# Optimization experiments

Measured on AMD Instinct MI355X. Metric: run time of the kernel, lower is better.

Reference implementation:

```python
import jax, jax.numpy as jnp
import numpy as np

N, E, H, FE, FV, L, FL, FO = 20000, 320000, 256, 64, 64, 4, 1024, 1


def setup_inputs() -> dict:
    key = jax.random.key(0)
    ks = jax.random.split(key, 28)
    s = 0.05
    rn = lambda k, shp: jax.random.normal(k, shp, jnp.float32) * s
    inp = {
        'x': jax.random.normal(ks[0], (N, FV), jnp.float32),
        'edge_attr': jax.random.normal(ks[1], (E, FE), jnp.float32),
        'edge_index': jax.random.randint(ks[2], (2, E), 0, N, jnp.int64) if False else jax.random.randint(ks[2], (2, E), 0, N),
        'ew': rn(ks[3], (H, FE)), 'eb': rn(ks[4], (H,)),
        'vw': rn(ks[5], (H, FV)), 'vb': rn(ks[6], (H,)),
        'Le_w': rn(ks[7], (L, H, H)), 'Le_b': rn(ks[8], (L, H)),
        'Lv_w': rn(ks[9], (L, H, H)), 'Lv_b': rn(ks[10], (L, H)),
        'bne_g': jnp.ones((L, H), jnp.float32), 'bne_b': jnp.zeros((L, H), jnp.float32),
        'bnv_g': jnp.ones((L, H), jnp.float32), 'bnv_b': jnp.zeros((L, H), jnp.float32),
        'gru_wih': rn(ks[11], (L, 3 * H, H)), 'gru_whh': rn(ks[12], (L, 3 * H, H)),
        'gru_bih': rn(ks[13], (L, 3 * H)), 'gru_bhh': rn(ks[14], (L, 3 * H)),
        'fin_w': rn(ks[15], (FL, H)), 'fin_b': rn(ks[16], (FL,)),
        'out_w': rn(ks[17], (FO, FL)), 'out_b': rn(ks[18], (FO,)),
    }
    return inp


def _bn(x, g, b):
    # BatchNorm1d, training-mode batch statistics (biased variance), eps=1e-5
    m = x.mean(axis=0)
    v = x.var(axis=0)
    return (x - m) * jax.lax.rsqrt(v + 1e-5) * g + b


def _forward(x, edge_attr, edge_index, ew, eb, vw, vb, Le_w, Le_b, Lv_w, Lv_b,
             bne_g, bne_b, bnv_g, bnv_b, gru_wih, gru_whh, gru_bih, gru_bhh,
             fin_w, fin_b, out_w, out_b):
    n_nodes = x.shape[0]
    num_layers = Le_w.shape[0]
    src, dst = edge_index[0], edge_index[1]
    seg = jnp.concatenate([src, dst])  # each edge contributes to both endpoints
    e_in = edge_attr @ ew.T + eb       # [E, H]
    v_in = x @ vw.T + vb               # [N, H]
    for k in range(num_layers):
        e = e_in @ Le_w[k].T + Le_b[k]
        vp = v_in @ Lv_w[k].T + Lv_b[k]
        ep = jax.nn.relu(_bn(e + vp[src] + vp[dst], bne_g[k], bne_b[k]))  # [E, H]
        # scatter-max of incident edge features into each vertex
        vie = jax.ops.segment_max(jnp.concatenate([ep, ep], axis=0), seg,
                                  num_segments=n_nodes)
        vie = jnp.where(jnp.isfinite(vie), vie, 0.0)  # isolated vertices -> 0
        # single-step GRU: input vie, hidden v_in
        gi = vie @ gru_wih[k].T + gru_bih[k]
        gh = v_in @ gru_whh[k].T + gru_bhh[k]
        ir, iz, ig = jnp.split(gi, 3, axis=1)
        hr, hz, hg = jnp.split(gh, 3, axis=1)
        r = jax.nn.sigmoid(ir + hr)
        z = jax.nn.sigmoid(iz + hz)
        n = jnp.tanh(ig + r * hg)
        h = (1.0 - z) * n + z * v_in
        v_c = jax.nn.relu(_bn(h, bnv_g[k], bnv_b[k]))
        v_in = v_c + v_in
        e_in = ep + e_in
    e_fin = e_in @ fin_w.T + fin_b
    return e_fin @ out_w.T + out_b  # [E, 1]


def reference(x, edge_attr, edge_index, ew, eb, vw, vb, Le_w, Le_b, Lv_w, Lv_b,
              bne_g, bne_b, bnv_g, bnv_b, gru_wih, gru_whh, gru_bih, gru_bhh,
              fin_w, fin_b, out_w, out_b):
    return _forward(x, edge_attr, edge_index, ew, eb, vw, vb, Le_w, Le_b, Lv_w,
                    Lv_b, bne_g, bne_b, bnv_g, bnv_b, gru_wih, gru_whh,
                    gru_bih, gru_bhh, fin_w, fin_b, out_w, out_b)
```

## Files before the change

### kernel.cpp

```cpp
#include <hip/hip_runtime.h>
#include <stdint.h>

constexpr int N  = 20000;
constexpr int E  = 320000;
constexpr int H  = 256;
constexpr int FEAT = 64;
constexpr int NL = 4;
constexpr int FL = 1024;
constexpr int NB_E = E / 32;

typedef unsigned short u16;
typedef short bf16x8 __attribute__((ext_vector_type(8)));
typedef float f32x4 __attribute__((ext_vector_type(4)));

__device__ __forceinline__ float bf2f(u16 u) {
    union { uint32_t i; float f; } v; v.i = ((uint32_t)u) << 16; return v.f;
}
__device__ __forceinline__ u16 f2bf(float f) {
    union { uint32_t i; float f; } v; v.f = f;
    uint32_t r = v.i + 0x7FFFu + ((v.i >> 16) & 1u);
    return (u16)(r >> 16);
}
__device__ __forceinline__ float sigmf(float x) { return 1.f / (1.f + __expf(-x)); }
__device__ __forceinline__ float tanhf_(float x) { return 2.f / (1.f + __expf(-2.f * x)) - 1.f; }

__device__ __forceinline__ unsigned int encf(float x) {
    unsigned int u = __float_as_uint(x);
    return (u & 0x80000000u) ? ~u : (u | 0x80000000u);
}
__device__ __forceinline__ float decf(unsigned int k) {
    unsigned int u = (k & 0x80000000u) ? (k ^ 0x80000000u) : ~k;
    return __uint_as_float(u);
}

template <bool W16>
__device__ __forceinline__ bf16x8 ldb(const u16* wb, const float* wf, size_t off) {
    if constexpr (W16) {
        return *(const bf16x8*)(wb + off);
    } else {
        float4 b0 = *(const float4*)(wf + off);
        float4 b1 = *(const float4*)(wf + off + 4);
        bf16x8 r;
        r[0] = (short)f2bf(b0.x); r[1] = (short)f2bf(b0.y);
        r[2] = (short)f2bf(b0.z); r[3] = (short)f2bf(b0.w);
        r[4] = (short)f2bf(b1.x); r[5] = (short)f2bf(b1.y);
        r[6] = (short)f2bf(b1.z); r[7] = (short)f2bf(b1.w);
        return r;
    }
}

__global__ void k_fuse_final(const float* __restrict__ fin_w, const float* __restrict__ fin_b,
                             const float* __restrict__ out_w, const float* __restrict__ out_b,
                             float* __restrict__ w_fo) {
    int h = threadIdx.x;
    float acc = 0.f;
    for (int f = 0; f < FL; ++f) acc = fmaf(out_w[f], fin_w[(size_t)f * H + h], acc);
    w_fo[h] = acc;
    if (h == 0) {
        float b = 0.f;
        for (int f = 0; f < FL; ++f) b = fmaf(out_w[f], fin_b[f], b);
        w_fo[H] = b + out_b[0];
    }
}

__global__ void k_cvt_w(const float* __restrict__ w, u16* __restrict__ o, int n4) {
    int i = blockIdx.x * 256 + threadIdx.x;
    if (i < n4) {
        float4 v = *(const float4*)(w + (size_t)i * 4);
        *(ushort4*)(o + (size_t)i * 4) = make_ushort4(f2bf(v.x), f2bf(v.y), f2bf(v.z), f2bf(v.w));
    }
}

__global__ void k_zero_int(int* __restrict__ p, int n) {
    int i = blockIdx.x * 256 + threadIdx.x;
    if (i < n) p[i] = 0;
}
__global__ void k_zero_f64(double* __restrict__ p, int n) {
    int i = blockIdx.x * 256 + threadIdx.x;
    if (i < n) p[i] = 0.0;
}
__global__ void k_hist2(const int* __restrict__ src, const int* __restrict__ dst,
                        int* __restrict__ curS, int* __restrict__ curD) {
    int e = blockIdx.x * 256 + threadIdx.x;
    if (e < E) { atomicAdd(&curS[src[e]], 1); atomicAdd(&curD[dst[e]], 1); }
}
__global__ void k_scan(int* __restrict__ cur) {
    __shared__ int cs[256];
    int t = threadIdx.x;
    constexpr int CH = (N + 255) / 256;
    int beg = t * CH, end = min(beg + CH, N);
    int s = 0;
    for (int i = beg; i < end; ++i) s += cur[i];
    cs[t] = s;
    __syncthreads();
    for (int off = 1; off < 256; off <<= 1) {
        int v = cs[t];
        int u = (t >= off) ? cs[t - off] : 0;
        __syncthreads();
        cs[t] = v + u;
        __syncthreads();
    }
    int run = (t > 0) ? cs[t - 1] : 0;
    for (int i = beg; i < end; ++i) { int d = cur[i]; cur[i] = run; run += d; }
}
__global__ void k_fill_perm(const int* __restrict__ src, const int* __restrict__ dst,
                            int* __restrict__ curS, int* __restrict__ curD,
                            int4* __restrict__ adjS, int4* __restrict__ sd2, int* __restrict__ pos) {
    int e = blockIdx.x * 256 + threadIdx.x;
    if (e < E) {
        int s = src[e], d = dst[e];
        int q = atomicAdd(&curD[d], 1);
        sd2[q] = make_int4(s, d, e, 0);
        pos[e] = q;
        int p = atomicAdd(&curS[s], 1);
        adjS[p] = make_int4(q, s, d, s);
    }
}
__global__ void k_fill_u32(unsigned int* __restrict__ p, unsigned int val) {
    size_t i = ((size_t)blockIdx.x * 256 + threadIdx.x) * 4;
    uint4 v = make_uint4(val, val, val, val);
    *(uint4*)(p + i) = v;
}

template <bool W16>
__global__ __launch_bounds__(256, 3) void k_proj_mfma(
    const float* __restrict__ A, const u16* __restrict__ wb, const float* __restrict__ wf,
    const float* __restrict__ bias, u16* __restrict__ C, int M, const int* __restrict__ perm)
{
    __shared__ u16 As[64][72];
    int t = threadIdx.x;
    int row0 = blockIdx.x * 64;
    int r = t >> 2, q = t & 3;
    if (row0 + r < M) {
        const float* gp = A + (size_t)(row0 + r) * FEAT + q * 16;
#pragma unroll
        for (int i = 0; i < 4; ++i) {
            float4 v = *(const float4*)(gp + i * 4);
            *(ushort4*)&As[r][q * 16 + i * 4] = make_ushort4(f2bf(v.x), f2bf(v.y), f2bf(v.z), f2bf(v.w));
        }
    } else {
#pragma unroll
        for (int i = 0; i < 4; ++i) *(ushort4*)&As[r][q * 16 + i * 4] = make_ushort4(0, 0, 0, 0);
    }
    __syncthreads();
    int w = t >> 6, l = t & 63, lane16 = l & 15, quad = l >> 4;
    f32x4 acc[4][4];
#pragma unroll
    for (int i = 0; i < 4; ++i)
#pragma unroll
        for (int j = 0; j < 4; ++j) acc[i][j] = (f32x4){0.f, 0.f, 0.f, 0.f};
#pragma unroll
    for (int k0 = 0; k0 < FEAT; k0 += 32) {
        bf16x8 a[4], b[4];
#pragma unroll
        for (int mt = 0; mt < 4; ++mt)
            a[mt] = *(const bf16x8*)&As[mt * 16 + lane16][k0 + quad * 8];
#pragma unroll
        for (int nt = 0; nt < 4; ++nt)
            b[nt] = ldb<W16>(wb, wf, (size_t)(w * 16 + nt * 64 + lane16) * FEAT + k0 + quad * 8);
#pragma unroll
        for (int mt = 0; mt < 4; ++mt)
#pragma unroll
            for (int nt = 0; nt < 4; ++nt)
                acc[mt][nt] = __builtin_amdgcn_mfma_f32_16x16x32_bf16(a[mt], b[nt], acc[mt][nt], 0, 0, 0);
    }
#pragma unroll
    for (int nt = 0; nt < 4; ++nt) {
        int col = w * 16 + nt * 64 + lane16;
        float bv = bias[col];
#pragma unroll
        for (int mt = 0; mt < 4; ++mt)
#pragma unroll
            for (int reg = 0; reg < 4; ++reg) {
                int row = mt * 16 + quad * 4 + reg;
                if (row0 + row < M) {
                    int pr = perm ? perm[row0 + row] : row0 + row;
                    C[(size_t)pr * H + col] = f2bf(acc[mt][nt][reg] + bv);
                }
            }
    }
}

template <bool W16>
__global__ __launch_bounds__(256, 2) void k_node_mfma(
    const u16* __restrict__ A, const u16* __restrict__ wb, const float* __restrict__ wf,
    u16* __restrict__ C)
{
    __shared__ u16 As[64][264];
    int t = threadIdx.x;
    int row0 = blockIdx.x * 64;
    int rows = min(64, N - row0);
    int r = t >> 2, q = t & 3;
    if (r < rows) {
        const u16* gp = A + (size_t)(row0 + r) * H + q * 64;
#pragma unroll
        for (int i = 0; i < 16; ++i)
            *(ushort4*)&As[r][q * 64 + i * 4] = *(const ushort4*)(gp + i * 4);
    } else {
#pragma unroll
        for (int i = 0; i < 16; ++i) *(ushort4*)&As[r][q * 64 + i * 4] = make_ushort4(0, 0, 0, 0);
    }
    __syncthreads();
    int w = t >> 6, l = t & 63, lane16 = l & 15, quad = l >> 4;
    f32x4 acc[4][4];
#pragma unroll
    for (int i = 0; i < 4; ++i)
#pragma unroll
        for (int j = 0; j < 4; ++j) acc[i][j] = (f32x4){0.f, 0.f, 0.f, 0.f};
    for (int k0 = 0; k0 < H; k0 += 32) {
        bf16x8 a[4], b[4];
#pragma unroll
        for (int mt = 0; mt < 4; ++mt)
            a[mt] = *(const bf16x8*)&As[mt * 16 + lane16][k0 + quad * 8];
#pragma unroll
        for (int nt = 0; nt < 4; ++nt)
            b[nt] = ldb<W16>(wb, wf, (size_t)(w * 16 + nt * 64 + lane16) * H + k0 + quad * 8);
#pragma unroll
        for (int mt = 0; mt < 4; ++mt)
#pragma unroll
            for (int nt = 0; nt < 4; ++nt)
                acc[mt][nt] = __builtin_amdgcn_mfma_f32_16x16x32_bf16(a[mt], b[nt], acc[mt][nt], 0, 0, 0);
    }
#pragma unroll
    for (int nt = 0; nt < 4; ++nt) {
        int col = w * 16 + nt * 64 + lane16;
#pragma unroll
        for (int mt = 0; mt < 4; ++mt)
#pragma unroll
            for (int reg = 0; reg < 4; ++reg) {
                int row = mt * 16 + quad * 4 + reg;
                if (row < rows)
                    C[(size_t)(row0 + row) * H + col] = f2bf(acc[mt][nt][reg]);
            }
    }
}

__global__ __launch_bounds__(256, 4) void k_edge_first(
    const u16* __restrict__ ein2, const u16* __restrict__ wbf,
    const u16* __restrict__ vp, const int4* __restrict__ sd2,
    const int* __restrict__ endo,
    unsigned int* __restrict__ vie, double* __restrict__ stats_e)
{
    __shared__ u16 As[32][264];
    __shared__ u16 Us[32][264];
    __shared__ int s_node[32];
    __shared__ int s_int[32];
    u16 (*praw)[264] = As;

    int t = threadIdx.x;
    int p0 = blockIdx.x * 32;
    int r = t >> 3, q = t & 7;
    {
        int4 en = sd2[p0 + r];
        const u16* gp = ein2 + (size_t)(p0 + r) * H + q * 32;
        const u16* vs = vp + (size_t)en.x * H + q * 32;
        const u16* vd = vp + (size_t)en.y * H + q * 32;
#pragma unroll
        for (int i = 0; i < 8; ++i)
            *(ushort4*)&As[r][q * 32 + i * 4] = *(const ushort4*)(gp + i * 4);
#pragma unroll
        for (int i = 0; i < 8; ++i) {
            ushort4 a4 = *(const ushort4*)(vs + i * 4);
            ushort4 b4 = *(const ushort4*)(vd + i * 4);
            *(ushort4*)&Us[r][q * 32 + i * 4] = make_ushort4(
                f2bf(bf2f(a4.x) + bf2f(b4.x)), f2bf(bf2f(a4.y) + bf2f(b4.y)),
                f2bf(bf2f(a4.z) + bf2f(b4.z)), f2bf(bf2f(a4.w) + bf2f(b4.w)));
        }
    }
    if (t < 32) {
        int nd = sd2[p0 + t].y;
        s_node[t] = nd;
        int st = (nd == 0) ? 0 : endo[nd - 1];
        int ee = endo[nd];
        s_int[t] = (st >= p0) && (ee <= p0 + 32);
    }
    __syncthreads();

    int w = t >> 6, l = t & 63, lane16 = l & 15, quad = l >> 4;
    f32x4 acc[2][4];
#pragma unroll
    for (int i = 0; i < 2; ++i)
#pragma unroll
        for (int j = 0; j < 4; ++j) acc[i][j] = (f32x4){0.f, 0.f, 0.f, 0.f};
    const u16* wb0 = wbf + (size_t)(w * 64 + lane16) * H + quad * 8;
    for (int k0 = 0; k0 < H; k0 += 32) {
        bf16x8 a[2], b[4];
#pragma unroll
        for (int mt = 0; mt < 2; ++mt)
            a[mt] = *(const bf16x8*)&As[mt * 16 + lane16][k0 + quad * 8];
#pragma unroll
        for (int nt = 0; nt < 4; ++nt)
            b[nt] = *(const bf16x8*)(wb0 + (size_t)nt * 16 * H + k0);
#pragma unroll
        for (int mt = 0; mt < 2; ++mt)
#pragma unroll
            for (int nt = 0; nt < 4; ++nt)
                acc[mt][nt] = __builtin_amdgcn_mfma_f32_16x16x32_bf16(a[mt], b[nt], acc[mt][nt], 0, 0, 0);
    }
    __syncthreads();

#pragma unroll
    for (int nt = 0; nt < 4; ++nt) {
        int col = w * 64 + nt * 16 + lane16;
        float s = 0.f, qq = 0.f;
#pragma unroll
        for (int mt = 0; mt < 2; ++mt)
#pragma unroll
            for (int reg = 0; reg < 4; ++reg) {
                int row = mt * 16 + quad * 4 + reg;
                float v = acc[mt][nt][reg] + bf2f(Us[row][col]);
                praw[row][col] = f2bf(v);
                s += v; qq += v * v;
            }
        s  += __shfl_xor(s, 16, 64);  s  += __shfl_xor(s, 32, 64);
        qq += __shfl_xor(qq, 16, 64); qq += __shfl_xor(qq, 32, 64);
        if (quad == 0) {
            int slice = blockIdx.x & 63;
            atomicAdd(&stats_e[(size_t)slice * 512 + col], (double)s);
            atomicAdd(&stats_e[(size_t)slice * 512 + 256 + col], (double)qq);
        }
    }
    __syncthreads();
    {
        int cur = s_node[0];
        float m = bf2f(praw[0][t]);
        for (int rr = 1; rr < 32; ++rr) {
            int nd = s_node[rr];
            float v = bf2f(praw[rr][t]);
            if (nd != cur) {
                if (s_int[rr - 1]) vie[(size_t)cur * H + t] = encf(m);
                else atomicMax(&vie[(size_t)cur * H + t], encf(m));
                cur = nd; m = v;
            } else m = fmaxf(m, v);
        }
        if (s_int[31]) vie[(size_t)cur * H + t] = encf(m);
        else atomicMax(&vie[(size_t)cur * H + t], encf(m));
    }
}

__global__ __launch_bounds__(256, 4) void k_edge_second(
    const u16* __restrict__ ein2, const u16* __restrict__ wbf,
    const u16* __restrict__ vp, const int4* __restrict__ adj,
    unsigned int* __restrict__ vie,
    const float* __restrict__ scale, const float* __restrict__ shift,
    u16* __restrict__ ein_rw)
{
    __shared__ u16 As[32][264];
    __shared__ u16 Us[32][264];
    __shared__ int s_pos[32];
    __shared__ int s_node[32];
    u16 (*praw)[264] = As;

    int t = threadIdx.x;
    int p0 = blockIdx.x * 32;
    int r = t >> 3, q = t & 7;
    {
        int4 en = adj[p0 + r];
        const u16* gp = ein2 + (size_t)en.x * H + q * 32;
        const u16* vs = vp + (size_t)en.y * H + q * 32;
        const u16* vd = vp + (size_t)en.z * H + q * 32;
#pragma unroll
        for (int i = 0; i < 8; ++i)
            *(ushort4*)&As[r][q * 32 + i * 4] = *(const ushort4*)(gp + i * 4);
#pragma unroll
        for (int i = 0; i < 8; ++i) {
            ushort4 a4 = *(const ushort4*)(vs + i * 4);
            ushort4 b4 = *(const ushort4*)(vd + i * 4);
            *(ushort4*)&Us[r][q * 32 + i * 4] = make_ushort4(
                f2bf(bf2f(a4.x) + bf2f(b4.x)), f2bf(bf2f(a4.y) + bf2f(b4.y)),
                f2bf(bf2f(a4.z) + bf2f(b4.z)), f2bf(bf2f(a4.w) + bf2f(b4.w)));
        }
    }
    if (t < 32) {
        int4 en = adj[p0 + t];
        s_pos[t] = en.x; s_node[t] = en.w;
    }
    __syncthreads();

    int w = t >> 6, l = t & 63, lane16 = l & 15, quad = l >> 4;
    f32x4 acc[2][4];
#pragma unroll
    for (int i = 0; i < 2; ++i)
#pragma unroll
        for (int j = 0; j < 4; ++j) acc[i][j] = (f32x4){0.f, 0.f, 0.f, 0.f};
    const u16* wb0 = wbf + (size_t)(w * 64 + lane16) * H + quad * 8;
    for (int k0 = 0; k0 < H; k0 += 32) {
        bf16x8 a[2], b[4];
#pragma unroll
        for (int mt = 0; mt < 2; ++mt)
            a[mt] = *(const bf16x8*)&As[mt * 16 + lane16][k0 + quad * 8];
#pragma unroll
        for (int nt = 0; nt < 4; ++nt)
            b[nt] = *(const bf16x8*)(wb0 + (size_t)nt * 16 * H + k0);
#pragma unroll
        for (int mt = 0; mt < 2; ++mt)
#pragma unroll
            for (int nt = 0; nt < 4; ++nt)
                acc[mt][nt] = __builtin_amdgcn_mfma_f32_16x16x32_bf16(a[mt], b[nt], acc[mt][nt], 0, 0, 0);
    }
    __syncthreads();

#pragma unroll
    for (int nt = 0; nt < 4; ++nt) {
        int col = w * 64 + nt * 16 + lane16;
#pragma unroll
        for (int mt = 0; mt < 2; ++mt)
#pragma unroll
            for (int reg = 0; reg < 4; ++reg) {
                int row = mt * 16 + quad * 4 + reg;
                praw[row][col] = f2bf(acc[mt][nt][reg] + bf2f(Us[row][col]));
            }
    }
    __syncthreads();
    {
        int cur = s_node[0];
        float m = bf2f(praw[0][t]);
        for (int rr = 1; rr < 32; ++rr) {
            int nd = s_node[rr];
            float v = bf2f(praw[rr][t]);
            if (nd != cur) {
                atomicMax(&vie[(size_t)cur * H + t], encf(m));
                cur = nd; m = v;
            } else m = fmaxf(m, v);
        }
        atomicMax(&vie[(size_t)cur * H + t], encf(m));
    }
    {
        u16* gp = ein_rw + (size_t)s_pos[r] * H + q * 32;
        const float* scp = scale + q * 32;
        const float* shp = shift + q * 32;
#pragma unroll
        for (int i = 0; i < 8; ++i) {
            int c = q * 32 + i * 4;
            ushort2 pa = *(const ushort2*)&praw[r][c];
            ushort2 pb = *(const ushort2*)&praw[r][c + 2];
            float4 sc = *(const float4*)(scp + i * 4);
            float4 sh = *(const float4*)(shp + i * 4);
            ushort4 ev = *(const ushort4*)(gp + i * 4);
            float o0 = bf2f(ev.x) + fmaxf(fmaf(bf2f(pa.x), sc.x, sh.x), 0.f);
            float o1 = bf2f(ev.y) + fmaxf(fmaf(bf2f(pa.y), sc.y, sh.y), 0.f);
            float o2 = bf2f(ev.z) + fmaxf(fmaf(bf2f(pb.x), sc.z, sh.z), 0.f);
            float o3 = bf2f(ev.w) + fmaxf(fmaf(bf2f(pb.y), sc.w, sh.w), 0.f);
            *(ushort4*)(gp + i * 4) = make_ushort4(f2bf(o0), f2bf(o1), f2bf(o2), f2bf(o3));
        }
    }
}

__global__ void k_bn_final_e(const double* __restrict__ stats_e,
                             const float* __restrict__ g, const float* __restrict__ b,
                             float* __restrict__ scale, float* __restrict__ shift) {
    int j = threadIdx.x;
    double m = 0.0, q = 0.0;
    for (int s = 0; s < 64; ++s) {
        m += stats_e[(size_t)s * 512 + j];
        q += stats_e[(size_t)s * 512 + 256 + j];
    }
    m /= (double)E;
    double var = q / (double)E - m * m;
    if (var < 0.0) var = 0.0;
    float inv = rsqrtf((float)var + 1e-5f);
    float sc = g[j] * inv;
    scale[j] = sc;
    shift[j] = b[j] - (float)m * sc;
}

__global__ void k_bn_final(const double* __restrict__ stats, int base,
                           const float* __restrict__ g, const float* __restrict__ b,
                           double cnt, float* __restrict__ scale, float* __restrict__ shift) {
    int j = threadIdx.x;
    double m = stats[base + j] / cnt;
    double var = stats[base + 256 + j] / cnt - m * m;
    if (var < 0.0) var = 0.0;
    float inv = rsqrtf((float)var + 1e-5f);
    float sc = g[j] * inv;
    scale[j] = sc;
    shift[j] = b[j] - (float)m * sc;
}

__global__ void k_vie_final(unsigned int* __restrict__ vie_u,
                            const float* __restrict__ scale, const float* __restrict__ shift) {
    size_t idx = ((size_t)blockIdx.x * 256 + threadIdx.x) * 4;
    int col = (int)(idx & (size_t)(H - 1));
    uint4 u = *(const uint4*)(vie_u + idx);
    float4 sc = *(const float4*)(scale + col);
    float4 sh = *(const float4*)(shift + col);
    float4 o;
    o.x = (u.x == 0u) ? 0.f : fmaxf(fmaf(decf(u.x), sc.x, sh.x), 0.f);
    o.y = (u.y == 0u) ? 0.f : fmaxf(fmaf(decf(u.y), sc.y, sh.y), 0.f);
    o.z = (u.z == 0u) ? 0.f : fmaxf(fmaf(decf(u.z), sc.z, sh.z), 0.f);
    o.w = (u.w == 0u) ? 0.f : fmaxf(fmaf(decf(u.w), sc.w, sh.w), 0.f);
    *(float4*)((float*)vie_u + idx) = o;
}

template <bool W16>
__global__ __launch_bounds__(256, 2) void k_gru_mfma(
    const float* __restrict__ vie, const u16* __restrict__ vin,
    const u16* __restrict__ wihb, const float* __restrict__ wihf,
    const u16* __restrict__ whhb, const float* __restrict__ whhf,
    const float* __restrict__ bih, const float* __restrict__ bhh,
    u16* __restrict__ hout, double* __restrict__ stats_v)
{
    __shared__ u16 Ae[64][264];
    __shared__ u16 Av[64][264];
    __shared__ float csum[256], csq[256];
    int t = threadIdx.x;
    int row0 = blockIdx.x * 64;
    int rows = min(64, N - row0);
    int r = t >> 2, q = t & 3;
    if (r < rows) {
        const float* gp = vie + (size_t)(row0 + r) * H + q * 64;
        const u16* hp = vin + (size_t)(row0 + r) * H + q * 64;
#pragma unroll
        for (int i = 0; i < 16; ++i) {
            float4 v = *(const float4*)(gp + i * 4);
            *(ushort4*)&Ae[r][q * 64 + i * 4] = make_ushort4(f2bf(v.x), f2bf(v.y), f2bf(v.z), f2bf(v.w));
            *(ushort4*)&Av[r][q * 64 + i * 4] = *(const ushort4*)(hp + i * 4);
        }
    } else {
#pragma unroll
        for (int i = 0; i < 16; ++i) {
            *(ushort4*)&Ae[r][q * 64 + i * 4] = make_ushort4(0, 0, 0, 0);
            *(ushort4*)&Av[r][q * 64 + i * 4] = make_ushort4(0, 0, 0, 0);
        }
    }
    __syncthreads();
    int w = t >> 6, l = t & 63, lane16 = l & 15, quad = l >> 4;

    for (int g = 0; g < 4; ++g) {
        int j = g * 64 + w * 16 + lane16;
        f32x4 aR[4], aZ[4], aIG[4], aHG[4];
#pragma unroll
        for (int mt = 0; mt < 4; ++mt) {
            aR[mt] = (f32x4){0.f, 0.f, 0.f, 0.f};  aZ[mt] = (f32x4){0.f, 0.f, 0.f, 0.f};
            aIG[mt] = (f32x4){0.f, 0.f, 0.f, 0.f}; aHG[mt] = (f32x4){0.f, 0.f, 0.f, 0.f};
        }
        for (int k0 = 0; k0 < H; k0 += 32) {
            size_t kq = (size_t)k0 + quad * 8;
            bf16x8 ae[4], av[4];
#pragma unroll
            for (int mt = 0; mt < 4; ++mt) {
                ae[mt] = *(const bf16x8*)&Ae[mt * 16 + lane16][k0 + quad * 8];
                av[mt] = *(const bf16x8*)&Av[mt * 16 + lane16][k0 + quad * 8];
            }
            bf16x8 bri = ldb<W16>(wihb, wihf, (size_t)j * H + kq);
            bf16x8 bzi = ldb<W16>(wihb, wihf, (size_t)(H + j) * H + kq);
            bf16x8 bgi = ldb<W16>(wihb, wihf, (size_t)(2 * H + j) * H + kq);
            bf16x8 brh = ldb<W16>(whhb, whhf, (size_t)j * H + kq);
            bf16x8 bzh = ldb<W16>(whhb, whhf, (size_t)(H + j) * H + kq);
            bf16x8 bgh = ldb<W16>(whhb, whhf, (size_t)(2 * H + j) * H + kq);
#pragma unroll
            for (int mt = 0; mt < 4; ++mt) {
                aR[mt]  = __builtin_amdgcn_mfma_f32_16x16x32_bf16(ae[mt], bri, aR[mt], 0, 0, 0);
                aR[mt]  = __builtin_amdgcn_mfma_f32_16x16x32_bf16(av[mt], brh, aR[mt], 0, 0, 0);
                aZ[mt]  = __builtin_amdgcn_mfma_f32_16x16x32_bf16(ae[mt], bzi, aZ[mt], 0, 0, 0);
                aZ[mt]  = __builtin_amdgcn_mfma_f32_16x16x32_bf16(av[mt], bzh, aZ[mt], 0, 0, 0);
                aIG[mt] = __builtin_amdgcn_mfma_f32_16x16x32_bf16(ae[mt], bgi, aIG[mt], 0, 0, 0);
                aHG[mt] = __builtin_amdgcn_mfma_f32_16x16x32_bf16(av[mt], bgh, aHG[mt], 0, 0, 0);
            }
        }
        float br_ = bih[j] + bhh[j];
        float bz_ = bih[H + j] + bhh[H + j];
        float bgi_ = bih[2 * H + j];
        float bgh_ = bhh[2 * H + j];
        float s = 0.f, qq = 0.f;
#pragma unroll
        for (int mt = 0; mt < 4; ++mt)
#pragma unroll
            for (int reg = 0; reg < 4; ++reg) {
                int row = mt * 16 + quad * 4 + reg;
                float rr = sigmf(aR[mt][reg] + br_);
                float zz = sigmf(aZ[mt][reg] + bz_);
                float nn = tanhf_(aIG[mt][reg] + bgi_ + rr * (aHG[mt][reg] + bgh_));
                float vv = bf2f(Av[row][j]);
                float hv = (1.f - zz) * nn + zz * vv;
                if (row < rows) {
                    hout[(size_t)(row0 + row) * H + j] = f2bf(hv);
                    s += hv; qq += hv * hv;
                }
            }
        s  += __shfl_xor(s, 16, 64);  s  += __shfl_xor(s, 32, 64);
        qq += __shfl_xor(qq, 16, 64); qq += __shfl_xor(qq, 32, 64);
        if (quad == 0) { csum[j] = s; csq[j] = qq; }
    }
    __syncthreads();
    atomicAdd(&stats_v[t], (double)csum[t]);
    atomicAdd(&stats_v[256 + t], (double)csq[t]);
}

__global__ void k_vertex_update(u16* __restrict__ vin, const u16* __restrict__ h,
                                const float* __restrict__ scale, const float* __restrict__ shift) {
    size_t idx = ((size_t)blockIdx.x * 256 + threadIdx.x) * 4;
    int col = (int)(idx & (size_t)(H - 1));
    ushort4 hv = *(const ushort4*)(h + idx);
    float4 sc = *(const float4*)(scale + col);
    float4 sh = *(const float4*)(shift + col);
    ushort4 vv = *(const ushort4*)(vin + idx);
    float o0 = bf2f(vv.x) + fmaxf(fmaf(bf2f(hv.x), sc.x, sh.x), 0.f);
    float o1 = bf2f(vv.y) + fmaxf(fmaf(bf2f(hv.y), sc.y, sh.y), 0.f);
    float o2 = bf2f(vv.z) + fmaxf(fmaf(bf2f(hv.z), sc.z, sh.z), 0.f);
    float o3 = bf2f(vv.w) + fmaxf(fmaf(bf2f(hv.w), sc.w, sh.w), 0.f);
    *(ushort4*)(vin + idx) = make_ushort4(f2bf(o0), f2bf(o1), f2bf(o2), f2bf(o3));
}

__global__ __launch_bounds__(256) void k_final(const u16* __restrict__ ein2,
                                               const int4* __restrict__ sd2,
                                               const float* __restrict__ w_fo, float* __restrict__ out) {
    int t = threadIdx.x;
    int lane = t & 63;
    int w = (blockIdx.x << 2) + (t >> 6);
    float4 wv = *(const float4*)(w_fo + lane * 4);
    float bfo = w_fo[H];
    int p0 = w * 64;
    for (int p = p0; p < p0 + 64; ++p) {
        ushort4 u = *(const ushort4*)(ein2 + (size_t)p * H + lane * 4);
        float s = bf2f(u.x) * wv.x + bf2f(u.y) * wv.y + bf2f(u.z) * wv.z + bf2f(u.w) * wv.w;
        for (int off = 32; off > 0; off >>= 1) s += __shfl_down(s, off, 64);
        if (lane == 0) out[sd2[p].z] = s + bfo;
    }
}

template <bool W16>
static void run_all(void* const* d_in, void* d_out, void* d_ws, hipStream_t stream) {
    const float* x         = (const float*)d_in[0];
    const float* edge_attr = (const float*)d_in[1];
    const int*   ei        = (const int*)d_in[2];
    const int*   src = ei;
    const int*   dst = ei + E;
    const float* ew  = (const float*)d_in[3];
    const float* eb  = (const float*)d_in[4];
    const float* vw  = (const float*)d_in[5];
    const float* vb  = (const float*)d_in[6];
    const float* Le_w = (const float*)d_in[7];
    const float* Lv_w = (const float*)d_in[9];
    const float* bne_g = (const float*)d_in[11];
    const float* bne_b = (const float*)d_in[12];
    const float* bnv_g = (const float*)d_in[13];
    const float* bnv_b = (const float*)d_in[14];
    const float* gwih  = (const float*)d_in[15];
    const float* gwhh  = (const float*)d_in[16];
    const float* gbih  = (const float*)d_in[17];
    const float* gbhh  = (const float*)d_in[18];
    const float* fin_w = (const float*)d_in[19];
    const float* fin_b = (const float*)d_in[20];
    const float* out_w = (const float*)d_in[21];
    const float* out_b = (const float*)d_in[22];
    float* out = (float*)d_out;

    const size_t nh = (size_t)N * H, eh = (size_t)E * H;
    char* base = (char*)d_ws;
    size_t off = 0;
    auto alloc = [&](size_t bytes) -> char* {
        char* p = base + off;
        off = (off + bytes + 255) & ~(size_t)255;
        return p;
    };
    float* w_fo = (float*)alloc((H + 1) * sizeof(float));
    u16* v_in = (u16*)alloc(nh * sizeof(u16));
    u16* vp   = (u16*)alloc(nh * sizeof(u16));
    unsigned int* vie_u = (unsigned int*)alloc(nh * sizeof(unsigned int));
    u16* e_in = (u16*)alloc(eh * sizeof(u16));
    u16* wbf  = (u16*)alloc((size_t)NL * H * H * sizeof(u16));
    double* stats_e = (double*)alloc((size_t)64 * 512 * sizeof(double));
    double* stats_v = (double*)alloc(512 * sizeof(double));
    float* scale_e = (float*)alloc(H * sizeof(float));
    float* shift_e = (float*)alloc(H * sizeof(float));
    float* scale_v = (float*)alloc(H * sizeof(float));
    float* shift_v = (float*)alloc(H * sizeof(float));
    int* curS = (int*)alloc((size_t)N * sizeof(int));
    int* curD = (int*)alloc((size_t)N * sizeof(int));
    int4* adjS = (int4*)alloc((size_t)E * sizeof(int4));
    int4* sd2  = (int4*)alloc((size_t)E * sizeof(int4));
    int*  pos  = (int*)alloc((size_t)E * sizeof(int));
    u16 *wbf_v = nullptr, *wbf_ih = nullptr, *wbf_hh = nullptr, *ew_b = nullptr, *vw_b = nullptr;
    if (W16) {
        wbf_v  = (u16*)alloc((size_t)NL * H * H * sizeof(u16));
        wbf_ih = (u16*)alloc((size_t)NL * 3 * H * H * sizeof(u16));
        wbf_hh = (u16*)alloc((size_t)NL * 3 * H * H * sizeof(u16));
        ew_b   = (u16*)alloc((size_t)H * FEAT * sizeof(u16));
        vw_b   = (u16*)alloc((size_t)H * FEAT * sizeof(u16));
    }
    u16* hbuf = vp;

    k_fuse_final<<<1, 256, 0, stream>>>(fin_w, fin_b, out_w, out_b, w_fo);
    k_cvt_w<<<(NL * H * H / 4 + 255) / 256, 256, 0, stream>>>(Le_w, wbf, NL * H * H / 4);
    if (W16) {
        k_cvt_w<<<(NL * H * H / 4 + 255) / 256, 256, 0, stream>>>(Lv_w, wbf_v, NL * H * H / 4);
        k_cvt_w<<<(NL * 3 * H * H / 4 + 255) / 256, 256, 0, stream>>>(gwih, wbf_ih, NL * 3 * H * H / 4);
        k_cvt_w<<<(NL * 3 * H * H / 4 + 255) / 256, 256, 0, stream>>>(gwhh, wbf_hh, NL * 3 * H * H / 4);
        k_cvt_w<<<(H * FEAT / 4 + 255) / 256, 256, 0, stream>>>(ew, ew_b, H * FEAT / 4);
        k_cvt_w<<<(H * FEAT / 4 + 255) / 256, 256, 0, stream>>>(vw, vw_b, H * FEAT / 4);
    }
    k_zero_int<<<(N + 255) / 256, 256, 0, stream>>>(curS, N);
    k_zero_int<<<(N + 255) / 256, 256, 0, stream>>>(curD, N);
    k_hist2<<<E / 256, 256, 0, stream>>>(src, dst, curS, curD);
    k_scan<<<1, 256, 0, stream>>>(curS);
    k_scan<<<1, 256, 0, stream>>>(curD);
    k_fill_perm<<<E / 256, 256, 0, stream>>>(src, dst, curS, curD, adjS, sd2, pos);
    const int ntile = (N + 63) / 64;
    k_proj_mfma<W16><<<ntile, 256, 0, stream>>>(x, vw_b, vw, vb, v_in, N, nullptr);
    k_proj_mfma<W16><<<E / 64, 256, 0, stream>>>(edge_attr, ew_b, ew, eb, e_in, E, pos);

    const int nstat = 64 * 512 + 512;
    for (int k = 0; k < NL; ++k) {
        k_zero_f64<<<(nstat + 255) / 256, 256, 0, stream>>>(stats_e, nstat);
        k_fill_u32<<<(int)(nh / 4 / 256), 256, 0, stream>>>(vie_u, 0u);
        k_node_mfma<W16><<<ntile, 256, 0, stream>>>(v_in,
            W16 ? wbf_v + (size_t)k * H * H : nullptr, Lv_w + (size_t)k * H * H, vp);
        k_edge_first<<<NB_E, 256, 0, stream>>>(e_in, wbf + (size_t)k * H * H, vp,
                                               sd2, curD, vie_u, stats_e);
        k_bn_final_e<<<1, 256, 0, stream>>>(stats_e, bne_g + k * H, bne_b + k * H, scale_e, shift_e);
        k_edge_second<<<NB_E, 256, 0, stream>>>(e_in, wbf + (size_t)k * H * H, vp,
                                                adjS, vie_u, scale_e, shift_e, e_in);
        k_vie_final<<<(int)(nh / 4 / 256), 256, 0, stream>>>(vie_u, scale_e, shift_e);
        k_gru_mfma<W16><<<ntile, 256, 0, stream>>>((const float*)vie_u, v_in,
            W16 ? wbf_ih + (size_t)k * 3 * H * H : nullptr, gwih + (size_t)k * 3 * H * H,
            W16 ? wbf_hh + (size_t)k * 3 * H * H : nullptr, gwhh + (size_t)k * 3 * H * H,
            gbih + (size_t)k * 3 * H, gbhh + (size_t)k * 3 * H, hbuf, stats_v);
        k_bn_final<<<1, 256, 0, stream>>>(stats_v, 0, bnv_g + k * H, bnv_b + k * H, (double)N, scale_v, shift_v);
        k_vertex_update<<<(int)(nh / 4 / 256), 256, 0, stream>>>(v_in, hbuf, scale_v, shift_v);
    }
    k_final<<<E / 256, 256, 0, stream>>>(e_in, sd2, w_fo, out);
}

extern "C" void kernel_launch(void* const* d_in, const int* in_sizes, int n_in,
                              void* d_out, int out_size, void* d_ws, size_t ws_size,
                              hipStream_t stream) {
    (void)in_sizes; (void)n_in; (void)out_size;
    const size_t nh = (size_t)N * H, eh = (size_t)E * H;
    auto rup = [](size_t x) { return (x + 255) & ~(size_t)255; };
    size_t need_base = rup((H + 1) * 4) + 2 * rup(nh * 2) + rup(nh * 4) + rup(eh * 2)
                     + rup((size_t)NL * H * H * 2) + rup((size_t)64 * 512 * 8) + rup(512 * 8)
                     + 4 * rup(H * 4) + 2 * rup((size_t)N * 4) + 2 * rup((size_t)E * 16)
                     + rup((size_t)E * 4);
    size_t need_w16 = rup((size_t)NL * H * H * 2)
                    + 2 * rup((size_t)NL * 3 * H * H * 2) + 2 * rup((size_t)H * FEAT * 2);
    if (ws_size == 0 || ws_size >= need_base + need_w16)
        run_all<true>(d_in, d_out, d_ws, stream);
    else
        run_all<false>(d_in, d_out, d_ws, stream);
}
```

Measured before the change: 3.030 ms.

## Double edge tile to 64 rows, pre-swizzle edge weights, shrink GRU tiles

Edge kernels now run 512 threads on 64-edge tiles, so each weight fragment is reused across twice as many rows. Each tile is handled as two independent 32-edge segments for the scatter-max, with the interior-segment test done per half. Edge weights are stored in a pre-swizzled MFMA fragment order for contiguous per-lane loads, and edge gathers use 16-byte vector loads. The GRU kernel switches to 32-row tiles with higher occupancy, which gives more blocks but less weight reuse per block.

```diff
diff --git a/kernel.cpp b/kernel.cpp
--- a/kernel.cpp
+++ b/kernel.cpp
@@ -7,7 +7,7 @@
 constexpr int FEAT = 64;
 constexpr int NL = 4;
 constexpr int FL = 1024;
-constexpr int NB_E = E / 32;
+constexpr int NB_E = E / 64;
 
 typedef unsigned short u16;
 typedef short bf16x8 __attribute__((ext_vector_type(8)));
@@ -31,6 +31,13 @@
 __device__ __forceinline__ float decf(unsigned int k) {
     unsigned int u = (k & 0x80000000u) ? (k ^ 0x80000000u) : ~k;
     return __uint_as_float(u);
+}
+__device__ __forceinline__ bf16x8 addbf8(bf16x8 a, bf16x8 b) {
+    bf16x8 o;
+#pragma unroll
+    for (int j = 0; j < 8; ++j)
+        o[j] = (short)f2bf(bf2f((u16)(unsigned short)a[j]) + bf2f((u16)(unsigned short)b[j]));
+    return o;
 }
 
 template <bool W16>
@@ -71,6 +78,22 @@
     }
 }
 
+__global__ void k_cvt_w_sw(const float* __restrict__ w, u16* __restrict__ o, int total) {
+    int i = blockIdx.x * 256 + threadIdx.x;
+    if (i >= total) return;
+    int l16 = i & 15;
+    int qd  = (i >> 4) & 3;
+    int ks  = (i >> 6) & 7;
+    int g   = (i >> 9) & 15;
+    int ly  = i >> 13;
+    int row = g * 16 + l16;
+    int k   = ks * 32 + qd * 8;
+    const float* src = w + ((size_t)ly * H + row) * H + k;
+    u16* dst = o + (size_t)i * 8;
+    *(ushort4*)dst       = make_ushort4(f2bf(src[0]), f2bf(src[1]), f2bf(src[2]), f2bf(src[3]));
+    *(ushort4*)(dst + 4) = make_ushort4(f2bf(src[4]), f2bf(src[5]), f2bf(src[6]), f2bf(src[7]));
+}
+
 __global__ void k_zero_int(int* __restrict__ p, int n) {
     int i = blockIdx.x * 256 + threadIdx.x;
     if (i < n) p[i] = 0;
@@ -235,20 +258,20 @@
     }
 }
 
-__global__ __launch_bounds__(256, 4) void k_edge_first(
-    const u16* __restrict__ ein2, const u16* __restrict__ wbf,
+__global__ __launch_bounds__(512, 4) void k_edge_first(
+    const u16* __restrict__ ein2, const u16* __restrict__ wsw,
     const u16* __restrict__ vp, const int4* __restrict__ sd2,
     const int* __restrict__ endo,
     unsigned int* __restrict__ vie, double* __restrict__ stats_e)
 {
-    __shared__ u16 As[32][264];
-    __shared__ u16 Us[32][264];
-    __shared__ int s_node[32];
-    __shared__ int s_int[32];
+    __shared__ u16 As[64][264];
+    __shared__ u16 Us[64][264];
+    __shared__ int s_node[64];
+    __shared__ int s_int[64];
     u16 (*praw)[264] = As;
 
     int t = threadIdx.x;
-    int p0 = blockIdx.x * 32;
+    int p0 = blockIdx.x * 64;
     int r = t >> 3, q = t & 7;
     {
         int4 en = sd2[p0 + r];
@@ -256,55 +279,55 @@
         const u16* vs = vp + (size_t)en.x * H + q * 32;
         const u16* vd = vp + (size_t)en.y * H + q * 32;
 #pragma unroll
-        for (int i = 0; i < 8; ++i)
-            *(ushort4*)&As[r][q * 32 + i * 4] = *(const ushort4*)(gp + i * 4);
-#pragma unroll
-        for (int i = 0; i < 8; ++i) {
-            ushort4 a4 = *(const ushort4*)(vs + i * 4);
-            ushort4 b4 = *(const ushort4*)(vd + i * 4);
-            *(ushort4*)&Us[r][q * 32 + i * 4] = make_ushort4(
-                f2bf(bf2f(a4.x) + bf2f(b4.x)), f2bf(bf2f(a4.y) + bf2f(b4.y)),
-                f2bf(bf2f(a4.z) + bf2f(b4.z)), f2bf(bf2f(a4.w) + bf2f(b4.w)));
-        }
-    }
-    if (t < 32) {
+        for (int i = 0; i < 4; ++i)
+            *(bf16x8*)&As[r][q * 32 + i * 8] = *(const bf16x8*)(gp + i * 8);
+#pragma unroll
+        for (int i = 0; i < 4; ++i) {
+            bf16x8 a8 = *(const bf16x8*)(vs + i * 8);
+            bf16x8 b8 = *(const bf16x8*)(vd + i * 8);
+            *(bf16x8*)&Us[r][q * 32 + i * 8] = addbf8(a8, b8);
+        }
+    }
+    if (t < 64) {
         int nd = sd2[p0 + t].y;
         s_node[t] = nd;
+        int seg0 = p0 + (t & 32);
         int st = (nd == 0) ? 0 : endo[nd - 1];
         int ee = endo[nd];
-        s_int[t] = (st >= p0) && (ee <= p0 + 32);
+        s_int[t] = (st >= seg0) && (ee <= seg0 + 32);
     }
     __syncthreads();
 
     int w = t >> 6, l = t & 63, lane16 = l & 15, quad = l >> 4;
-    f32x4 acc[2][4];
-#pragma unroll
-    for (int i = 0; i < 2; ++i)
-#pragma unroll
-        for (int j = 0; j < 4; ++j) acc[i][j] = (f32x4){0.f, 0.f, 0.f, 0.f};
-    const u16* wb0 = wbf + (size_t)(w * 64 + lane16) * H + quad * 8;
-    for (int k0 = 0; k0 < H; k0 += 32) {
-        bf16x8 a[2], b[4];
-#pragma unroll
-        for (int mt = 0; mt < 2; ++mt)
+    f32x4 acc[4][2];
+#pragma unroll
+    for (int i = 0; i < 4; ++i)
+#pragma unroll
+        for (int j = 0; j < 2; ++j) acc[i][j] = (f32x4){0.f, 0.f, 0.f, 0.f};
+    int woff = (quad * 16 + lane16) * 8;
+    for (int ks = 0; ks < 8; ++ks) {
+        int k0 = ks * 32;
+        bf16x8 a[4], b[2];
+#pragma unroll
+        for (int mt = 0; mt < 4; ++mt)
             a[mt] = *(const bf16x8*)&As[mt * 16 + lane16][k0 + quad * 8];
 #pragma unroll
-        for (int nt = 0; nt < 4; ++nt)
-            b[nt] = *(const bf16x8*)(wb0 + (size_t)nt * 16 * H + k0);
-#pragma unroll
-        for (int mt = 0; mt < 2; ++mt)
-#pragma unroll
-            for (int nt = 0; nt < 4; ++nt)
+        for (int nt = 0; nt < 2; ++nt)
+            b[nt] = *(const bf16x8*)(wsw + (size_t)(w * 2 + nt) * 4096 + ks * 512 + woff);
+#pragma unroll
+        for (int mt = 0; mt < 4; ++mt)
+#pragma unroll
+            for (int nt = 0; nt < 2; ++nt)
                 acc[mt][nt] = __builtin_amdgcn_mfma_f32_16x16x32_bf16(a[mt], b[nt], acc[mt][nt], 0, 0, 0);
     }
     __syncthreads();
 
 #pragma unroll
-    for (int nt = 0; nt < 4; ++nt) {
-        int col = w * 64 + nt * 16 + lane16;
+    for (int nt = 0; nt < 2; ++nt) {
+        int col = w * 32 + nt * 16 + lane16;
         float s = 0.f, qq = 0.f;
 #pragma unroll
-        for (int mt = 0; mt < 2; ++mt)
+        for (int mt = 0; mt < 4; ++mt)
 #pragma unroll
             for (int reg = 0; reg < 4; ++reg) {
                 int row = mt * 16 + quad * 4 + reg;
@@ -322,37 +345,39 @@
     }
     __syncthreads();
     {
-        int cur = s_node[0];
-        float m = bf2f(praw[0][t]);
+        int seg = t >> 8, col = t & 255;
+        int base = seg * 32;
+        int cur = s_node[base];
+        float m = bf2f(praw[base][col]);
         for (int rr = 1; rr < 32; ++rr) {
-            int nd = s_node[rr];
-            float v = bf2f(praw[rr][t]);
+            int nd = s_node[base + rr];
+            float v = bf2f(praw[base + rr][col]);
             if (nd != cur) {
-                if (s_int[rr - 1]) vie[(size_t)cur * H + t] = encf(m);
-                else atomicMax(&vie[(size_t)cur * H + t], encf(m));
+                if (s_int[base + rr - 1]) vie[(size_t)cur * H + col] = encf(m);
+                else atomicMax(&vie[(size_t)cur * H + col], encf(m));
                 cur = nd; m = v;
             } else m = fmaxf(m, v);
         }
-        if (s_int[31]) vie[(size_t)cur * H + t] = encf(m);
-        else atomicMax(&vie[(size_t)cur * H + t], encf(m));
-    }
-}
-
-__global__ __launch_bounds__(256, 4) void k_edge_second(
-    const u16* __restrict__ ein2, const u16* __restrict__ wbf,
+        if (s_int[base + 31]) vie[(size_t)cur * H + col] = encf(m);
+        else atomicMax(&vie[(size_t)cur * H + col], encf(m));
+    }
+}
+
+__global__ __launch_bounds__(512, 4) void k_edge_second(
+    const u16* __restrict__ ein2, const u16* __restrict__ wsw,
     const u16* __restrict__ vp, const int4* __restrict__ adj,
     unsigned int* __restrict__ vie,
     const float* __restrict__ scale, const float* __restrict__ shift,
     u16* __restrict__ ein_rw)
 {
-    __shared__ u16 As[32][264];
-    __shared__ u16 Us[32][264];
-    __shared__ int s_pos[32];
-    __shared__ int s_node[32];
+    __shared__ u16 As[64][264];
+    __shared__ u16 Us[64][264];
+    __shared__ int s_pos[64];
+    __shared__ int s_node[64];
     u16 (*praw)[264] = As;
 
     int t = threadIdx.x;
-    int p0 = blockIdx.x * 32;
+    int p0 = blockIdx.x * 64;
     int r = t >> 3, q = t & 7;
     {
         int4 en = adj[p0 + r];
@@ -360,51 +385,50 @@
         const u16* vs = vp + (size_t)en.y * H + q * 32;
         const u16* vd = vp + (size_t)en.z * H + q * 32;
 #pragma unroll
-        for (int i = 0; i < 8; ++i)
-            *(ushort4*)&As[r][q * 32 + i * 4] = *(const ushort4*)(gp + i * 4);
-#pragma unroll
-        for (int i = 0; i < 8; ++i) {
-            ushort4 a4 = *(const ushort4*)(vs + i * 4);
-            ushort4 b4 = *(const ushort4*)(vd + i * 4);
-            *(ushort4*)&Us[r][q * 32 + i * 4] = make_ushort4(
-                f2bf(bf2f(a4.x) + bf2f(b4.x)), f2bf(bf2f(a4.y) + bf2f(b4.y)),
-                f2bf(bf2f(a4.z) + bf2f(b4.z)), f2bf(bf2f(a4.w) + bf2f(b4.w)));
-        }
-    }
-    if (t < 32) {
+        for (int i = 0; i < 4; ++i)
+            *(bf16x8*)&As[r][q * 32 + i * 8] = *(const bf16x8*)(gp + i * 8);
+#pragma unroll
+        for (int i = 0; i < 4; ++i) {
+            bf16x8 a8 = *(const bf16x8*)(vs + i * 8);
+            bf16x8 b8 = *(const bf16x8*)(vd + i * 8);
+            *(bf16x8*)&Us[r][q * 32 + i * 8] = addbf8(a8, b8);
+        }
+    }
+    if (t < 64) {
         int4 en = adj[p0 + t];
         s_pos[t] = en.x; s_node[t] = en.w;
     }
     __syncthreads();
 
     int w = t >> 6, l = t & 63, lane16 = l & 15, quad = l >> 4;
-    f32x4 acc[2][4];
-#pragma unroll
-    for (int i = 0; i < 2; ++i)
-#pragma unroll
-        for (int j = 0; j < 4; ++j) acc[i][j] = (f32x4){0.f, 0.f, 0.f, 0.f};
-    const u16* wb0 = wbf + (size_t)(w * 64 + lane16) * H + quad * 8;
-    for (int k0 = 0; k0 < H; k0 += 32) {
-        bf16x8 a[2], b[4];
-#pragma unroll
-        for (int mt = 0; mt < 2; ++mt)
+    f32x4 acc[4][2];
+#pragma unroll
+    for (int i = 0; i < 4; ++i)
+#pragma unroll
+        for (int j = 0; j < 2; ++j) acc[i][j] = (f32x4){0.f, 0.f, 0.f, 0.f};
+    int woff = (quad * 16 + lane16) * 8;
+    for (int ks = 0; ks < 8; ++ks) {
+        int k0 = ks * 32;
+        bf16x8 a[4], b[2];
+#pragma unroll
+        for (int mt = 0; mt < 4; ++mt)
             a[mt] = *(const bf16x8*)&As[mt * 16 + lane16][k0 + quad * 8];
 #pragma unroll
-        for (int nt = 0; nt < 4; ++nt)
-            b[nt] = *(const bf16x8*)(wb0 + (size_t)nt * 16 * H + k0);
-#pragma unroll
-        for (int mt = 0; mt < 2; ++mt)
-#pragma unroll
-            for (int nt = 0; nt < 4; ++nt)
+        for (int nt = 0; nt < 2; ++nt)
+            b[nt] = *(const bf16x8*)(wsw + (size_t)(w * 2 + nt) * 4096 + ks * 512 + woff);
+#pragma unroll
+        for (int mt = 0; mt < 4; ++mt)
+#pragma unroll
+            for (int nt = 0; nt < 2; ++nt)
                 acc[mt][nt] = __builtin_amdgcn_mfma_f32_16x16x32_bf16(a[mt], b[nt], acc[mt][nt], 0, 0, 0);
     }
     __syncthreads();
 
 #pragma unroll
-    for (int nt = 0; nt < 4; ++nt) {
-        int col = w * 64 + nt * 16 + lane16;
-#pragma unroll
-        for (int mt = 0; mt < 2; ++mt)
+    for (int nt = 0; nt < 2; ++nt) {
+        int col = w * 32 + nt * 16 + lane16;
+#pragma unroll
+        for (int mt = 0; mt < 4; ++mt)
 #pragma unroll
             for (int reg = 0; reg < 4; ++reg) {
                 int row = mt * 16 + quad * 4 + reg;
@@ -413,17 +437,19 @@
     }
     __syncthreads();
     {
-        int cur = s_node[0];
-        float m = bf2f(praw[0][t]);
+        int seg = t >> 8, col = t & 255;
+        int base = seg * 32;
+        int cur = s_node[base];
+        float m = bf2f(praw[base][col]);
         for (int rr = 1; rr < 32; ++rr) {
-            int nd = s_node[rr];
-            float v = bf2f(praw[rr][t]);
+            int nd = s_node[base + rr];
+            float v = bf2f(praw[base + rr][col]);
             if (nd != cur) {
-                atomicMax(&vie[(size_t)cur * H + t], encf(m));
+                atomicMax(&vie[(size_t)cur * H + col], encf(m));
                 cur = nd; m = v;
             } else m = fmaxf(m, v);
         }
-        atomicMax(&vie[(size_t)cur * H + t], encf(m));
+        atomicMax(&vie[(size_t)cur * H + col], encf(m));
     }
     {
         u16* gp = ein_rw + (size_t)s_pos[r] * H + q * 32;
@@ -493,34 +519,36 @@
 }
 
 template <bool W16>
-__global__ __launch_bounds__(256, 2) void k_gru_mfma(
+__global__ __launch_bounds__(256, 3) void k_gru_mfma(
     const float* __restrict__ vie, const u16* __restrict__ vin,
     const u16* __restrict__ wihb, const float* __restrict__ wihf,
     const u16* __restrict__ whhb, const float* __restrict__ whhf,
     const float* __restrict__ bih, const float* __restrict__ bhh,
     u16* __restrict__ hout, double* __restrict__ stats_v)
 {
-    __shared__ u16 Ae[64][264];
-    __shared__ u16 Av[64][264];
+    __shared__ u16 Ae[32][264];
+    __shared__ u16 Av[32][264];
     __shared__ float csum[256], csq[256];
     int t = threadIdx.x;
-    int row0 = blockIdx.x * 64;
-    int rows = min(64, N - row0);
-    int r = t >> 2, q = t & 3;
+    int row0 = blockIdx.x * 32;
+    int rows = min(32, N - row0);
+    int r = t >> 3, q = t & 7;
     if (r < rows) {
-        const float* gp = vie + (size_t)(row0 + r) * H + q * 64;
-        const u16* hp = vin + (size_t)(row0 + r) * H + q * 64;
-#pragma unroll
-        for (int i = 0; i < 16; ++i) {
+        const float* gp = vie + (size_t)(row0 + r) * H + q * 32;
+        const u16* hp = vin + (size_t)(row0 + r) * H + q * 32;
+#pragma unroll
+        for (int i = 0; i < 8; ++i) {
             float4 v = *(const float4*)(gp + i * 4);
-            *(ushort4*)&Ae[r][q * 64 + i * 4] = make_ushort4(f2bf(v.x), f2bf(v.y), f2bf(v.z), f2bf(v.w));
-            *(ushort4*)&Av[r][q * 64 + i * 4] = *(const ushort4*)(hp + i * 4);
-        }
+            *(ushort4*)&Ae[r][q * 32 + i * 4] = make_ushort4(f2bf(v.x), f2bf(v.y), f2bf(v.z), f2bf(v.w));
+        }
+#pragma unroll
+        for (int i = 0; i < 4; ++i)
+            *(bf16x8*)&Av[r][q * 32 + i * 8] = *(const bf16x8*)(hp + i * 8);
     } else {
 #pragma unroll
-        for (int i = 0; i < 16; ++i) {
-            *(ushort4*)&Ae[r][q * 64 + i * 4] = make_ushort4(0, 0, 0, 0);
-            *(ushort4*)&Av[r][q * 64 + i * 4] = make_ushort4(0, 0, 0, 0);
+        for (int i = 0; i < 8; ++i) {
+            *(ushort4*)&Ae[r][q * 32 + i * 4] = make_ushort4(0, 0, 0, 0);
+            *(ushort4*)&Av[r][q * 32 + i * 4] = make_ushort4(0, 0, 0, 0);
         }
     }
     __syncthreads();
@@ -528,17 +556,17 @@
 
     for (int g = 0; g < 4; ++g) {
         int j = g * 64 + w * 16 + lane16;
-        f32x4 aR[4], aZ[4], aIG[4], aHG[4];
-#pragma unroll
-        for (int mt = 0; mt < 4; ++mt) {
+        f32x4 aR[2], aZ[2], aIG[2], aHG[2];
+#pragma unroll
+        for (int mt = 0; mt < 2; ++mt) {
             aR[mt] = (f32x4){0.f, 0.f, 0.f, 0.f};  aZ[mt] = (f32x4){0.f, 0.f, 0.f, 0.f};
             aIG[mt] = (f32x4){0.f, 0.f, 0.f, 0.f}; aHG[mt] = (f32x4){0.f, 0.f, 0.f, 0.f};
         }
         for (int k0 = 0; k0 < H; k0 += 32) {
             size_t kq = (size_t)k0 + quad * 8;
-            bf16x8 ae[4], av[4];
-#pragma unroll
-            for (int mt = 0; mt < 4; ++mt) {
+            bf16x8 ae[2], av[2];
+#pragma unroll
+            for (int mt = 0; mt < 2; ++mt) {
                 ae[mt] = *(const bf16x8*)&Ae[mt * 16 + lane16][k0 + quad * 8];
                 av[mt] = *(const bf16x8*)&Av[mt * 16 + lane16][k0 + quad * 8];
             }
@@ -549,7 +577,7 @@
             bf16x8 bzh = ldb<W16>(whhb, whhf, (size_t)(H + j) * H + kq);
             bf16x8 bgh = ldb<W16>(whhb, whhf, (size_t)(2 * H + j) * H + kq);
 #pragma unroll
-            for (int mt = 0; mt < 4; ++mt) {
+            for (int mt = 0; mt < 2; ++mt) {
                 aR[mt]  = __builtin_amdgcn_mfma_f32_16x16x32_bf16(ae[mt], bri, aR[mt], 0, 0, 0);
                 aR[mt]  = __builtin_amdgcn_mfma_f32_16x16x32_bf16(av[mt], brh, aR[mt], 0, 0, 0);
                 aZ[mt]  = __builtin_amdgcn_mfma_f32_16x16x32_bf16(ae[mt], bzi, aZ[mt], 0, 0, 0);
@@ -564,7 +592,7 @@
         float bgh_ = bhh[2 * H + j];
         float s = 0.f, qq = 0.f;
 #pragma unroll
-        for (int mt = 0; mt < 4; ++mt)
+        for (int mt = 0; mt < 2; ++mt)
 #pragma unroll
             for (int reg = 0; reg < 4; ++reg) {
                 int row = mt * 16 + quad * 4 + reg;
@@ -682,7 +710,7 @@
     u16* hbuf = vp;
 
     k_fuse_final<<<1, 256, 0, stream>>>(fin_w, fin_b, out_w, out_b, w_fo);
-    k_cvt_w<<<(NL * H * H / 4 + 255) / 256, 256, 0, stream>>>(Le_w, wbf, NL * H * H / 4);
+    k_cvt_w_sw<<<(NL * H * H / 8 + 255) / 256, 256, 0, stream>>>(Le_w, wbf, NL * H * H / 8);
     if (W16) {
         k_cvt_w<<<(NL * H * H / 4 + 255) / 256, 256, 0, stream>>>(Lv_w, wbf_v, NL * H * H / 4);
         k_cvt_w<<<(NL * 3 * H * H / 4 + 255) / 256, 256, 0, stream>>>(gwih, wbf_ih, NL * 3 * H * H / 4);
@@ -701,18 +729,19 @@
     k_proj_mfma<W16><<<E / 64, 256, 0, stream>>>(edge_attr, ew_b, ew, eb, e_in, E, pos);
 
     const int nstat = 64 * 512 + 512;
+    const int gtile = (N + 31) / 32;
     for (int k = 0; k < NL; ++k) {
         k_zero_f64<<<(nstat + 255) / 256, 256, 0, stream>>>(stats_e, nstat);
         k_fill_u32<<<(int)(nh / 4 / 256), 256, 0, stream>>>(vie_u, 0u);
         k_node_mfma<W16><<<ntile, 256, 0, stream>>>(v_in,
             W16 ? wbf_v + (size_t)k * H * H : nullptr, Lv_w + (size_t)k * H * H, vp);
-        k_edge_first<<<NB_E, 256, 0, stream>>>(e_in, wbf + (size_t)k * H * H, vp,
+        k_edge_first<<<NB_E, 512, 0, stream>>>(e_in, wbf + (size_t)k * H * H, vp,
                                                sd2, curD, vie_u, stats_e);
         k_bn_final_e<<<1, 256, 0, stream>>>(stats_e, bne_g + k * H, bne_b + k * H, scale_e, shift_e);
-        k_edge_second<<<NB_E, 256, 0, stream>>>(e_in, wbf + (size_t)k * H * H, vp,
+        k_edge_second<<<NB_E, 512, 0, stream>>>(e_in, wbf + (size_t)k * H * H, vp,
                                                 adjS, vie_u, scale_e, shift_e, e_in);
         k_vie_final<<<(int)(nh / 4 / 256), 256, 0, stream>>>(vie_u, scale_e, shift_e);
-        k_gru_mfma<W16><<<ntile, 256, 0, stream>>>((const float*)vie_u, v_in,
+        k_gru_mfma<W16><<<gtile, 256, 0, stream>>>((const float*)vie_u, v_in,
             W16 ? wbf_ih + (size_t)k * 3 * H * H : nullptr, gwih + (size_t)k * 3 * H * H,
             W16 ? wbf_hh + (size_t)k * 3 * H * H : nullptr, gwhh + (size_t)k * 3 * H * H,
             gbih + (size_t)k * 3 * H, gbhh + (size_t)k * 3 * H, hbuf, stats_v);
```

Result: faster. 2.444 ms (-19.4%).
